# Kernel tuning notes

Measured on AMD Instinct MI355X. Metric: run time of the kernel, lower is better.

The kernel has to match this reference:

```python
import jax, jax.numpy as jnp
import numpy as np

B, T = 2, 2048
DENSE = 1024
SPARSE = 1024
NH = 8
HD = SPARSE // NH          # 128
WINDOW = 64
K = 32
RANK = HD // 4             # 32
GATE_THRESH = 0.2


def setup_inputs() -> dict:
    key = jax.random.key(0)
    ks = jax.random.split(key, 12)
    return {
        "x": jax.random.normal(ks[0], (B, T, DENSE), dtype=jnp.float32),
        "enc_q": jax.random.normal(ks[1], (NH, DENSE, HD), dtype=jnp.float32) * 0.02,
        "enc_v": jax.random.normal(ks[2], (NH, DENSE, HD), dtype=jnp.float32) * 0.02,
        # metric network: Linear(SPARSE, SPARSE//2) -> GELU -> Linear(SPARSE//2, NH*HD)
        "metric_w1": jax.random.normal(ks[3], (SPARSE, SPARSE // 2), dtype=jnp.float32) * (1.0 / np.sqrt(SPARSE)),
        "metric_b1": jnp.zeros((SPARSE // 2,), dtype=jnp.float32),
        "metric_w2": jax.random.normal(ks[4], (SPARSE // 2, NH * HD), dtype=jnp.float32) * (1.0 / np.sqrt(SPARSE // 2)),
        "metric_b2": jnp.zeros((NH * HD,), dtype=jnp.float32),
        "base_metric": jnp.ones((NH, HD), dtype=jnp.float32) * 0.1,
        "hebb_U": jax.random.normal(ks[5], (NH, HD, RANK), dtype=jnp.float32) * 0.01,
        "hebb_V": jax.random.normal(ks[6], (NH, RANK, HD), dtype=jnp.float32) * 0.01,
        "decoder": jax.random.normal(ks[7], (NH * HD, DENSE), dtype=jnp.float32) * 0.02,
    }


def _causal_window_indices(t_len, window):
    pos = jnp.arange(t_len)
    off = jnp.arange(window)
    idx = jnp.clip(pos[:, None] - off[None, :], 0, t_len - 1)  # (T, W)
    mask = idx <= pos[:, None]
    return idx, mask


def _dynamic_metric(field, w1, b1, w2, b2, base):
    # field: (B, T, SPARSE)
    sig = field.mean(axis=1)
    if field.shape[1] >= 8:
        sig = sig + field[:, ::8].mean(axis=1) * 0.5
    h = jax.nn.gelu(sig @ w1 + b1, approximate=False)
    mod = (h @ w2 + b2).reshape(field.shape[0], NH, HD)
    return jax.nn.softplus(base[None] + 0.1 * mod)  # (B, NH, HD)


def reference(x, enc_q, enc_v, metric_w1, metric_b1, metric_w2, metric_b2,
              base_metric, hebb_U, hebb_V, decoder):
    Bb, Tt, _ = x.shape
    query_sparse = jax.nn.relu(jnp.einsum('btd,nde->btne', x, enc_q))  # (B,T,NH,HD)
    value_sparse = jax.nn.relu(jnp.einsum('btd,nde->btne', x, enc_v))

    metric = _dynamic_metric(query_sparse.reshape(Bb, Tt, NH * HD),
                             metric_w1, metric_b1, metric_w2, metric_b2, base_metric)

    idx, mask = _causal_window_indices(Tt, WINDOW)  # (T,W)
    idx_b = jnp.broadcast_to(idx[None], (Bb, Tt, WINDOW))
    batch_ix = jnp.arange(Bb)[:, None, None]

    outs = []
    for h in range(NH):
        q_h = query_sparse[:, :, h, :]   # (B,T,HD)
        v_h = value_sparse[:, :, h, :]
        m_h = metric[:, h][:, None, None, :]  # (B,1,1,HD)

        k_windows = q_h[:, idx, :]            # (B,T,W,HD) gather
        diff = k_windows - q_h[:, :, None, :]
        dist = jnp.sqrt((diff * diff * m_h).sum(axis=-1) + 1e-8)  # (B,T,W)
        dist = jnp.where(mask[None], dist, jnp.inf)

        neg_d, loc = jax.lax.top_k(-dist, K)  # smallest-K distances
        topd = -neg_d
        top_idx = jnp.take_along_axis(idx_b, loc, axis=2)  # (B,T,K)

        infl = jnp.exp(-topd)
        infl = infl / (infl.sum(axis=-1, keepdims=True) + 1e-8)

        neighbor_v = v_h[batch_ix, top_idx]   # (B,T,K,HD)
        context = jnp.einsum('btk,btkd->btd', infl, neighbor_v)

        q_norm = jnp.linalg.norm(q_h, axis=-1, keepdims=True)
        gate = (q_norm > GATE_THRESH).astype(q_h.dtype)
        heb_mat = hebb_U[h] @ hebb_V[h]       # (HD,HD)
        q_unit = q_h / jnp.maximum(q_norm, 1e-12)  # F.normalize
        heb_ctx = q_unit @ heb_mat
        context = context + gate * 0.1 * heb_ctx

        outs.append(q_h * context)

    out_sparse = jnp.stack(outs, axis=2)           # (B,T,NH,HD)
    return out_sparse.reshape(Bb, Tt, NH * HD) @ decoder
```

## Files before the change

### kernel.cpp

```cpp
#include <hip/hip_runtime.h>
#include <math.h>

#define T_ 2048
#define NH_ 8
#define HD_ 128

typedef unsigned short u16;
typedef short bf16x8 __attribute__((ext_vector_type(8)));
typedef _Float16 f16x8 __attribute__((ext_vector_type(8)));
typedef float f32x4 __attribute__((ext_vector_type(4)));

union FH { _Float16 h; u16 u; };

__device__ __forceinline__ u16 f2h(float f)
{
    FH c; c.h = (_Float16)f; return c.u;
}
__device__ __forceinline__ float h2f(u16 v)
{
    FH c; c.u = v; return (float)c.h;
}
__device__ __forceinline__ void split1h(float f, u16& h, u16& l)
{
    h = f2h(f);
    l = f2h(f - h2f(h));
}

__device__ __forceinline__ u16 f2bf(float f)
{
    unsigned u = __float_as_uint(f);
    return (u16)((u + 0x7FFFu + ((u >> 16) & 1u)) >> 16);
}
__device__ __forceinline__ float bf2f(u16 h)
{
    return __uint_as_float(((unsigned)h) << 16);
}


__global__ __launch_bounds__(256) void cvt_in(const float* __restrict__ x,
                                              const float* __restrict__ enc_q,
                                              const float* __restrict__ enc_v,
                                              u16* __restrict__ xh,
                                              u16* __restrict__ WTh)
{
    __shared__ u16 tH[32][33];
    const int bid = blockIdx.x;
    if (bid < 4096) {
        int i = (bid * 256 + threadIdx.x) * 4;
        int m = i >> 10, k = i & 1023;
        float4 v = *(const float4*)&x[i];
        ushort4 hv = {f2h(v.x), f2h(v.y), f2h(v.z), f2h(v.w)};
        long o = (long)(m >> 6) * 65536 + (k >> 5) * 2048
               + ((k >> 3) & 3) * 512 + (m & 63) * 8 + (k & 7);
        *(ushort4*)&xh[o] = hv;
    } else {
        int rb = bid - 4096;
        int bx = rb & 31, by = (rb >> 5) & 31, bz = rb >> 10;
        const float* Bw = bz ? enc_v : enc_q;
        const int nofs = bz << 10;
        const int tid = threadIdx.x;
        const int tx = tid & 31, ty = tid >> 5;
        const int k0 = bx * 32, c0 = by * 32;
        #pragma unroll
        for (int r = 0; r < 4; ++r) {
            int k = k0 + ty * 4 + r;
            int c = c0 + tx;
            float v = Bw[(long)(c >> 7) * 131072 + (long)k * 128 + (c & 127)];
            tH[ty * 4 + r][tx] = f2h(v);
        }
        __syncthreads();
        #pragma unroll
        for (int r = 0; r < 4; ++r) {
            int n = nofs + c0 + ty * 4 + r;
            int k = k0 + tx;
            long o = (long)(n >> 6) * 65536 + (k >> 5) * 2048
                   + ((k >> 3) & 3) * 512 + (n & 63) * 8 + (k & 7);
            WTh[o] = tH[tx][ty * 4 + r];
        }
    }
}

__global__ __launch_bounds__(256) void cvt_wT_pk(const float* __restrict__ src0,
                                                 u16* __restrict__ WTh,
                                                 int Kd, int cs, int cm, long sn, int sk)
{
    __shared__ u16 tH[32][33];
    const float* Bw = src0;
    const int tid = threadIdx.x;
    const int tx = tid & 31, ty = tid >> 5;
    const int k0 = blockIdx.x * 32, c0 = blockIdx.y * 32;
    #pragma unroll
    for (int r = 0; r < 4; ++r) {
        int k = k0 + ty * 4 + r;
        int c = c0 + tx;
        float v = Bw[(long)(c >> cs) * sn + (long)k * sk + (c & cm)];
        tH[ty * 4 + r][tx] = f2h(v);
    }
    __syncthreads();
    const long sstr = (long)Kd * 64;
    #pragma unroll
    for (int r = 0; r < 4; ++r) {
        int n = c0 + ty * 4 + r;
        int k = k0 + tx;
        long o = (long)(n >> 6) * sstr + (k >> 5) * 2048
               + ((k >> 3) & 3) * 512 + (n & 63) * 8 + (k & 7);
        WTh[o] = tH[tx][ty * 4 + r];
    }
}

__global__ __launch_bounds__(256, 1) void gemm_qv(
    const u16* __restrict__ Ah, const u16* __restrict__ Bh,
    float* __restrict__ Qf, u16* __restrict__ Vh,
    float* __restrict__ Ps, float* __restrict__ Ps8, int Kd)
{
    __shared__ __align__(16) u16 S[4][6144];

    const int tid  = threadIdx.x;
    const int w    = tid >> 6;
    const int lane = tid & 63;

    const int id   = blockIdx.x;
    const int m0   = (id & 31) * 128;
    const int n0   = (id >> 5) * 256;

    const int mw   = (w & 1) * 64, nw = (w >> 1) * 128;
    const int mr   = lane & 15, quad = lane >> 4;

    const long sstr = (long)Kd * 64;
    const u16* gAh = Ah + (long)((m0 + mw) >> 6) * sstr;
    const u16* gB0 = Bh + (long)((n0 + nw) >> 6) * sstr;
    const u16* gB1 = gB0 + sstr;

    u16* W = &S[w][0];

    f32x4 acc[4][8] = {};
    uint4 a0, a1, a2, a3;
    uint4 b0, b1, b2, b3, b4, b5, b6, b7;

#define LOADG(KT) do { long t = (long)(KT) * 2048 + lane * 8;                        \
    a0 = *(const uint4*)(gAh + t +    0); a1 = *(const uint4*)(gAh + t +  512);      \
    a2 = *(const uint4*)(gAh + t + 1024); a3 = *(const uint4*)(gAh + t + 1536);      \
    b0 = *(const uint4*)(gB0 + t +    0); b1 = *(const uint4*)(gB0 + t +  512);      \
    b2 = *(const uint4*)(gB0 + t + 1024); b3 = *(const uint4*)(gB0 + t + 1536);      \
    b4 = *(const uint4*)(gB1 + t +    0); b5 = *(const uint4*)(gB1 + t +  512);      \
    b6 = *(const uint4*)(gB1 + t + 1024); b7 = *(const uint4*)(gB1 + t + 1536); } while (0)

#define STOREG() do { u16* D = W + lane * 8;                                         \
    *(uint4*)(D +    0) = a0; *(uint4*)(D +  512) = a1;                              \
    *(uint4*)(D + 1024) = a2; *(uint4*)(D + 1536) = a3;                              \
    *(uint4*)(D + 2048) = b0; *(uint4*)(D + 2560) = b1;                              \
    *(uint4*)(D + 3072) = b2; *(uint4*)(D + 3584) = b3;                              \
    *(uint4*)(D + 4096) = b4; *(uint4*)(D + 4608) = b5;                              \
    *(uint4*)(D + 5120) = b6; *(uint4*)(D + 5632) = b7; } while (0)

    LOADG(0);
    STOREG();
    LOADG(1);

    const int NT = Kd >> 5;
    for (int kt = 0; kt < NT; ++kt) {
        f16x8 fah[4], fbh[8];
        #pragma unroll
        for (int i = 0; i < 4; ++i)
            fah[i] = *(const f16x8*)(W + quad * 512 + (i * 16 + mr) * 8);
        #pragma unroll
        for (int j = 0; j < 8; ++j)
            fbh[j] = *(const f16x8*)(W + 2048 + ((j < 4) ? 0 : 2048)
                                     + quad * 512 + ((j & 3) * 16 + mr) * 8);
        if (kt + 1 < NT) STOREG();
        if (kt + 2 < NT) LOADG(kt + 2);
        #pragma unroll
        for (int i = 0; i < 4; ++i)
            #pragma unroll
            for (int j = 0; j < 8; ++j)
                acc[i][j] = __builtin_amdgcn_mfma_f32_16x16x32_f16(fah[i], fbh[j], acc[i][j], 0, 0, 0);
    }
#undef LOADG
#undef STOREG

    if (n0 < 1024) {
        #pragma unroll
        for (int i = 0; i < 4; ++i)
            #pragma unroll
            for (int j = 0; j < 8; ++j)
                #pragma unroll
                for (int r = 0; r < 4; ++r) {
                    float v = fmaxf(acc[i][j][r], 0.f);
                    acc[i][j][r] = v;
                    int row = m0 + mw + i * 16 + quad * 4 + r;
                    int col = n0 + nw + j * 16 + mr;
                    Qf[(long)row * 1024 + col] = v;
                }
        int slot = (id & 31) * 2 + (w & 1);
        #pragma unroll
        for (int j = 0; j < 8; ++j) {
            float ps = 0.f, p8 = 0.f;
            #pragma unroll
            for (int i = 0; i < 4; ++i) {
                #pragma unroll
                for (int r = 0; r < 4; ++r) ps += acc[i][j][r];
                if ((quad & 1) == 0) p8 += acc[i][j][0];
            }
            ps += __shfl_xor(ps, 16, 64); ps += __shfl_xor(ps, 32, 64);
            p8 += __shfl_xor(p8, 16, 64); p8 += __shfl_xor(p8, 32, 64);
            if (quad == 0) {
                int col = n0 + nw + j * 16 + mr;
                Ps [slot * 1024 + col] = ps;
                Ps8[slot * 1024 + col] = p8;
            }
        }
    } else {
        #pragma unroll
        for (int i = 0; i < 4; ++i)
            #pragma unroll
            for (int j = 0; j < 8; ++j)
                #pragma unroll
                for (int r = 0; r < 4; ++r) {
                    float v = fmaxf(acc[i][j][r], 0.f);
                    int row = m0 + mw + i * 16 + quad * 4 + r;
                    int col = n0 - 1024 + nw + j * 16 + mr;
                    Vh[(long)row * 1024 + col] = f2h(v);
                }
    }
}

__global__ __launch_bounds__(256, 1) void gemm_dec(
    const u16* __restrict__ Ah, const u16* __restrict__ Bh,
    float* __restrict__ C, int N, int Kd)
{
    __shared__ __align__(16) u16 S[4][4096];

    const int tid  = threadIdx.x;
    const int w    = tid >> 6;
    const int lane = tid & 63;

    const int id   = blockIdx.x;
    const int m0   = (((id & 7) << 2) + ((id >> 3) & 3)) * 128;
    const int n0   = (id >> 5) * 128;

    const int mw   = (w & 1) * 64, nw = (w >> 1) * 64;
    const int mr   = lane & 15, quad = lane >> 4;

    const long sstr = (long)Kd * 64;
    const u16* gAh = Ah + (long)((m0 + mw) >> 6) * sstr;
    const u16* gBh = Bh + (long)((n0 + nw) >> 6) * sstr;

    u16* W = &S[w][0];

    f32x4 acc[4][4] = {};
    uint4 a0, a1, a2, a3, b0, b1, b2, b3;

#define LOADG(KT) do { long t = (long)(KT) * 2048 + lane * 8;                        \
    a0 = *(const uint4*)(gAh + t +    0); a1 = *(const uint4*)(gAh + t +  512);      \
    a2 = *(const uint4*)(gAh + t + 1024); a3 = *(const uint4*)(gAh + t + 1536);      \
    b0 = *(const uint4*)(gBh + t +    0); b1 = *(const uint4*)(gBh + t +  512);      \
    b2 = *(const uint4*)(gBh + t + 1024); b3 = *(const uint4*)(gBh + t + 1536); } while (0)

#define STOREG() do { u16* D = W + lane * 8;                                         \
    *(uint4*)(D +    0) = a0; *(uint4*)(D +  512) = a1;                              \
    *(uint4*)(D + 1024) = a2; *(uint4*)(D + 1536) = a3;                              \
    *(uint4*)(D + 2048) = b0; *(uint4*)(D + 2560) = b1;                              \
    *(uint4*)(D + 3072) = b2; *(uint4*)(D + 3584) = b3; } while (0)

    LOADG(0);
    STOREG();
    LOADG(1);

    const int NT = Kd >> 5;
    for (int kt = 0; kt < NT; ++kt) {
        f16x8 fah[4], fbh[4];
        #pragma unroll
        for (int i = 0; i < 4; ++i) {
            int ro = quad * 512 + (i * 16 + mr) * 8;
            fah[i] = *(const f16x8*)(W + ro);
            fbh[i] = *(const f16x8*)(W + 2048 + ro);
        }
        if (kt + 1 < NT) STOREG();
        if (kt + 2 < NT) LOADG(kt + 2);
        #pragma unroll
        for (int i = 0; i < 4; ++i)
            #pragma unroll
            for (int j = 0; j < 4; ++j)
                acc[i][j] = __builtin_amdgcn_mfma_f32_16x16x32_f16(fah[i], fbh[j], acc[i][j], 0, 0, 0);
    }
#undef LOADG
#undef STOREG

    #pragma unroll
    for (int i = 0; i < 4; ++i)
        #pragma unroll
        for (int j = 0; j < 4; ++j)
            #pragma unroll
            for (int r = 0; r < 4; ++r) {
                int row = m0 + mw + i * 16 + quad * 4 + r;
                int col = n0 + nw + j * 16 + mr;
                C[(long)row * N + col] = acc[i][j][r];
            }
}

__global__ __launch_bounds__(256) void heb_gemm(
    const u16* __restrict__ Qbf, const u16* __restrict__ MhT,
    u16* __restrict__ HEBbf)
{
    __shared__ __align__(16) u16 sA[4][128][8], sB[4][128][8];

    const int tid  = threadIdx.x;
    const int w    = tid >> 6;
    const int lane = tid & 63;
    const int m0   = blockIdx.x * 128;
    const int h    = blockIdx.y;
    const int mw   = w * 32;
    const int mr   = lane & 15, quad = lane >> 4;
    const u16* Bm  = MhT + h * 16384;

    f32x4 acc[2][8] = {};

    for (int k0 = 0; k0 < 128; k0 += 32) {
        #pragma unroll
        for (int u = 0; u < 4; ++u) {
            int c = (w & 1) * 4 + u;
            int kq = c >> 1, half = c & 1;
            const u16* src; u16* dst; long gofs;
            if (w < 2) {
                src = Qbf;
                dst = &sA[0][0][0] + kq * 1024 + half * 512;
                gofs = (long)(m0 + half * 64 + lane) * 1024 + h * 128 + k0 + kq * 8;
            } else {
                src = Bm;
                dst = &sB[0][0][0] + kq * 1024 + half * 512;
                gofs = (long)(half * 64 + lane) * 128 + k0 + kq * 8;
            }
            __builtin_amdgcn_global_load_lds(
                (const __attribute__((address_space(1))) unsigned int*)(src + gofs),
                (__attribute__((address_space(3))) unsigned int*)dst, 16, 0, 0);
        }
        __syncthreads();

        bf16x8 fa[2], fb[8];
        #pragma unroll
        for (int i = 0; i < 2; ++i)
            fa[i] = *(const bf16x8*)&sA[quad][mw + i * 16 + mr][0];
        #pragma unroll
        for (int j = 0; j < 8; ++j)
            fb[j] = *(const bf16x8*)&sB[quad][j * 16 + mr][0];
        #pragma unroll
        for (int i = 0; i < 2; ++i)
            #pragma unroll
            for (int j = 0; j < 8; ++j)
                acc[i][j] = __builtin_amdgcn_mfma_f32_16x16x32_bf16(fa[i], fb[j], acc[i][j], 0, 0, 0);
        __syncthreads();
    }

    #pragma unroll
    for (int i = 0; i < 2; ++i)
        #pragma unroll
        for (int j = 0; j < 8; ++j)
            #pragma unroll
            for (int r = 0; r < 4; ++r) {
                int row = m0 + mw + i * 16 + quad * 4 + r;
                int col = h * 128 + j * 16 + mr;
                HEBbf[(long)row * 1024 + col] = f2bf(acc[i][j][r]);
            }
}

__global__ __launch_bounds__(256) void qu_stage(const float* __restrict__ Qf,
                                                const float* __restrict__ Me,
                                                u16* __restrict__ Qbf,
                                                u16* __restrict__ Uh, u16* __restrict__ Ul,
                                                float* __restrict__ nArr)
{
    int gid4 = (blockIdx.x * 256 + threadIdx.x) * 4;
    int e4 = gid4 & 127;
    int t  = (gid4 >> 7) & 2047;
    int bh = gid4 >> 18;
    int b  = bh >> 3, h = bh & 7;
    float4 q = *(const float4*)&Qf[((long)(b * 2048 + t)) * 1024 + h * 128 + e4];
    ushort4 qo = {f2bf(q.x), f2bf(q.y), f2bf(q.z), f2bf(q.w)};
    *(ushort4*)&Qbf[((long)(b * 2048 + t)) * 1024 + h * 128 + e4] = qo;

    float4 m = *(const float4*)&Me[bh * 128 + e4];
    float ux = sqrtf(m.x) * q.x, uy = sqrtf(m.y) * q.y;
    float uz = sqrtf(m.z) * q.z, uw = sqrtf(m.w) * q.w;
    u16 h0, l0, h1, l1, h2, l2, h3, l3;
    split1h(ux, h0, l0); split1h(uy, h1, l1);
    split1h(uz, h2, l2); split1h(uw, h3, l3);
    ushort4 hv = {h0, h1, h2, h3}, lv = {l0, l1, l2, l3};
    *(ushort4*)&Uh[gid4] = hv;
    *(ushort4*)&Ul[gid4] = lv;
    float ps = ux * ux + uy * uy + uz * uz + uw * uw;
    #pragma unroll
    for (int mm = 16; mm; mm >>= 1) ps += __shfl_xor(ps, mm, 64);
    if ((threadIdx.x & 31) == 0) nArr[gid4 >> 7] = ps;
}

__global__ __launch_bounds__(256, 1) void dist_gemm(
    const u16* __restrict__ Uh, const u16* __restrict__ Ul,
    const float* __restrict__ nArr, float* __restrict__ band)
{
    __shared__ __align__(16) u16 sAh[4][64][8],  sAl[4][64][8];
    __shared__ __align__(16) u16 sBh[4][128][8], sBl[4][128][8];
    __shared__ float epi[4][16][128];

    const int tid  = threadIdx.x;
    const int w    = tid >> 6;
    const int lane = tid & 63;
    const int mr   = lane & 15, quad = lane >> 4;
    const int bid  = blockIdx.x;
    const int tile = bid & 31, bh = bid >> 5;
    const int t0   = tile * 64;
    const long ub  = (long)bh * 2048 * 128;

    const u16 *s0, *s1, *s2, *s3, *s4, *s5;
    u16 *d0, *d1, *d2, *d3, *d4, *d5;
    long o0, o1, o2, o3, o4, o5;
    {
        auto mk = [&](int i, const u16*& src, u16*& dst, long& ofs) {
            int c = i * 256 + tid;
            if (c < 512) {
                int row = c & 63, kq = (c >> 6) & 3;
                src = (c < 256) ? Uh : Ul;
                ofs = ub + (long)(t0 + row) * 128 + kq * 8;
                dst = ((c < 256) ? &sAh[0][0][0] : &sAl[0][0][0]) + kq * 512 + row * 8;
            } else {
                int cb = c - 512;
                int row = cb & 127, kq = (cb >> 7) & 3;
                src = (cb < 512) ? Uh : Ul;
                ofs = ub + (long)(t0 - 64 + row) * 128 + kq * 8;
                dst = ((cb < 512) ? &sBh[0][0][0] : &sBl[0][0][0]) + kq * 1024 + row * 8;
            }
        };
        mk(0, s0, d0, o0); mk(1, s1, d1, o1); mk(2, s2, d2, o2);
        mk(3, s3, d3, o3); mk(4, s4, d4, o4); mk(5, s5, d5, o5);
    }

    f32x4 acc[8] = {};
    uint4 g0, g1, g2, g3, g4, g5;
    g0 = *(const uint4*)(s0 + o0); g1 = *(const uint4*)(s1 + o1);
    g2 = *(const uint4*)(s2 + o2); g3 = *(const uint4*)(s3 + o3);
    g4 = *(const uint4*)(s4 + o4); g5 = *(const uint4*)(s5 + o5);

    for (int k0 = 0; k0 < 128; k0 += 32) {
        *(uint4*)d0 = g0; *(uint4*)d1 = g1; *(uint4*)d2 = g2;
        *(uint4*)d3 = g3; *(uint4*)d4 = g4; *(uint4*)d5 = g5;
        __syncthreads();

        if (k0 + 32 < 128) {
            int kn = k0 + 32;
            g0 = *(const uint4*)(s0 + o0 + kn); g1 = *(const uint4*)(s1 + o1 + kn);
            g2 = *(const uint4*)(s2 + o2 + kn); g3 = *(const uint4*)(s3 + o3 + kn);
            g4 = *(const uint4*)(s4 + o4 + kn); g5 = *(const uint4*)(s5 + o5 + kn);
        }

        f16x8 fah = *(const f16x8*)&sAh[quad][w * 16 + mr][0];
        f16x8 fal = *(const f16x8*)&sAl[quad][w * 16 + mr][0];
        #pragma unroll
        for (int j = 0; j < 8; ++j) {
            f16x8 fbh = *(const f16x8*)&sBh[quad][j * 16 + mr][0];
            f16x8 fbl = *(const f16x8*)&sBl[quad][j * 16 + mr][0];
            acc[j] = __builtin_amdgcn_mfma_f32_16x16x32_f16(fah, fbh, acc[j], 0, 0, 0);
            acc[j] = __builtin_amdgcn_mfma_f32_16x16x32_f16(fah, fbl, acc[j], 0, 0, 0);
            acc[j] = __builtin_amdgcn_mfma_f32_16x16x32_f16(fal, fbh, acc[j], 0, 0, 0);
        }
        __syncthreads();
    }

    #pragma unroll
    for (int j = 0; j < 8; ++j)
        #pragma unroll
        for (int r = 0; r < 4; ++r)
            epi[w][quad * 4 + r][j * 16 + mr] = acc[j][r];
    __syncthreads();

    const float* nb = nArr + (long)bh * 2048;
    #pragma unroll
    for (int i = 0; i < 16; ++i) {
        int id = i * 256 + tid;
        int tl = id >> 6, j = id & 63;
        int t  = t0 + tl;
        int r  = t - j;
        int rc = r < 0 ? 0 : r;
        int rl = tl - j + 64;
        float S  = epi[tl >> 4][tl & 15][rl];
        float d2 = nb[t] + nb[rc] - 2.0f * S;
        band[((long)bh * 2048 + t) * 64 + j] = d2;
    }
}

__global__ __launch_bounds__(256) void mlp1_part(const float* __restrict__ Ps,
                                                 const float* __restrict__ Ps8,
                                                 const float* __restrict__ w1,
                                                 float* __restrict__ Pm)
{
    __shared__ float ssig[32];
    int tid = threadIdx.x;
    int o  = blockIdx.x * 256 + tid;
    int b  = blockIdx.y;
    int kc = blockIdx.z;
    int k0 = kc * 32;
    if (tid < 32) {
        int k = k0 + tid;
        float s = 0.f, s8 = 0.f;
        #pragma unroll
        for (int ms = 0; ms < 32; ++ms) {
            long po = ((long)(b * 32 + ms)) * 1024 + k;
            s  += Ps[po];
            s8 += Ps8[po];
        }
        ssig[tid] = s * (1.0f / 2048.0f) + 0.5f * s8 * (1.0f / 256.0f);
    }
    __syncthreads();
    float a = 0.f;
    #pragma unroll 8
    for (int kk = 0; kk < 32; ++kk)
        a += ssig[kk] * w1[(long)(k0 + kk) * 512 + o];
    Pm[((b * 32) + kc) * 512 + o] = a;
}

__global__ __launch_bounds__(256) void mlp2_part(const float* __restrict__ Pm1,
                                                 const float* __restrict__ b1,
                                                 const float* __restrict__ w2,
                                                 float* __restrict__ Pm)
{
    __shared__ float sH[32];
    int tid = threadIdx.x;
    int c  = blockIdx.x * 256 + tid;
    int b  = blockIdx.y;
    int kc = blockIdx.z;
    int k0 = kc * 32;
    if (tid < 32) {
        int o = k0 + tid;
        float a = b1[o];
        #pragma unroll
        for (int kcc = 0; kcc < 32; ++kcc)
            a += Pm1[(b * 32 + kcc) * 512 + o];
        sH[tid] = 0.5f * a * (1.0f + erff(a * 0.70710678118f));
    }
    __syncthreads();
    float a = 0.f;
    #pragma unroll 8
    for (int kk = 0; kk < 32; ++kk)
        a += sH[kk] * w2[(long)(k0 + kk) * 1024 + c];
    Pm[((b * 16) + kc) * 1024 + c] = a;
}

__global__ __launch_bounds__(256) void mlp2fin_hebb(
    const float* __restrict__ Pm, const float* __restrict__ b2,
    const float* __restrict__ base, float* __restrict__ metric,
    const float* __restrict__ U, const float* __restrict__ Vh,
    u16* __restrict__ MhT)
{
    int id = blockIdx.x;
    if (id < 8) {
        int c = (id & 3) * 256 + threadIdx.x;
        int b = id >> 2;
        float a = b2[c];
        #pragma unroll
        for (int kc = 0; kc < 16; ++kc)
            a += Pm[(b * 16 + kc) * 1024 + c];
        float mv = base[c] + 0.1f * a;
        metric[b * 1024 + c] = fmaxf(mv, 0.f) + log1pf(expf(-fabsf(mv)));
    } else {
        int gid = (id - 8) * 256 + threadIdx.x;
        int h = gid >> 14;
        int rem = gid & 16383;
        int e = rem >> 7;
        int f = rem & 127;
        float a = 0.f;
        #pragma unroll
        for (int r = 0; r < 32; ++r)
            a += U[(h * 128 + f) * 32 + r] * Vh[(h * 32 + r) * 128 + e];
        MhT[(h * 128 + e) * 128 + f] = f2bf(a);
    }
}

__global__ __launch_bounds__(256) void context_k(
    const float* __restrict__ Qf, const u16* __restrict__ Vh,
    const float* __restrict__ band, const u16* __restrict__ HEBbf,
    u16* __restrict__ CTh)
{
    __shared__ float wv[4][32];
    __shared__ int   wi[4][32];

    const int w    = threadIdx.x >> 6;
    const int lane = threadIdx.x & 63;
    const int gw   = blockIdx.x * 4 + w;
    const int h    = gw & 7;
    const int bt   = gw >> 3;
    const int t    = bt & (T_ - 1);
    const int b    = bt >> 11;
    const int bh   = b * 8 + h;

    const long qrow  = (long)bt * 1024 + h * 128;
    const long hrow  = (long)bt * 1024 + h * 128;

    float q0 = Qf[qrow + lane], q1 = Qf[qrow + 64 + lane];
    float ss = q0 * q0 + q1 * q1;
    #pragma unroll
    for (int s = 32; s; s >>= 1) ss += __shfl_xor(ss, s, 64);
    const float qn  = sqrtf(ss);
    const float inv = 1.0f / fmaxf(qn, 1e-12f);

    int je = lane < t ? lane : t;
    float d2v = (je == 0) ? 0.f
              : band[((long)bh * 2048 + t) * 64 + je];
    float d2f = fmaxf(d2v, 0.f) + 1e-8f;
    unsigned kb = (__float_as_uint(d2f) & 0xFFFFFFC0u) | (unsigned)lane;

    #pragma unroll
    for (int k = 2; k <= 32; k <<= 1)
        #pragma unroll
        for (int s = k >> 1; s >= 1; s >>= 1) {
            unsigned ok = __shfl_xor(kb, s, 64);
            bool takeMin = (((lane & k) == 0) == ((lane & s) == 0));
            if ((ok < kb) == takeMin) kb = ok;
        }
    {
        unsigned ok = __shfl_xor(kb, 32, 64);
        kb = ok < kb ? ok : kb;
    }

    int jj = kb & 63;
    float wexp = 0.f;
    if (lane < 32)
        wexp = expf(-sqrtf(__uint_as_float(kb & 0xFFFFFFC0u)));
    float tot = wexp;
    #pragma unroll
    for (int s = 32; s; s >>= 1) tot += __shfl_xor(tot, s, 64);
    float wn = wexp / (tot + 1e-8f);
    if (lane < 32) {
        wv[w][lane] = wn;
        int ii = t - jj; if (ii < 0) ii = 0;
        wi[w][lane] = ii;
    }

    float c0 = 0.f, c1 = 0.f;
    #pragma unroll 8
    for (int k = 0; k < 32; ++k) {
        float wk = wv[w][k];
        long vb = ((long)(b * T_ + wi[w][k])) * 1024 + h * 128;
        c0 += wk * h2f(Vh[vb + lane]);
        c1 += wk * h2f(Vh[vb + 64 + lane]);
    }

    if (qn > 0.2f) {
        float s = 0.1f * inv;
        c0 += s * bf2f(HEBbf[hrow + lane]);
        c1 += s * bf2f(HEBbf[hrow + 64 + lane]);
    }

    int c0c = h * 128 + lane, c1c = c0c + 64;
    long po0 = (long)(bt >> 6) * 65536 + (c0c >> 5) * 2048
             + ((c0c >> 3) & 3) * 512 + (bt & 63) * 8 + (c0c & 7);
    long po1 = (long)(bt >> 6) * 65536 + (c1c >> 5) * 2048
             + ((c1c >> 3) & 3) * 512 + (bt & 63) * 8 + (c1c & 7);
    CTh[po0] = f2h(q0 * c0);
    CTh[po1] = f2h(q1 * c1);
}

extern "C" void kernel_launch(void* const* d_in, const int* in_sizes, int n_in,
                              void* d_out, int out_size, void* d_ws, size_t ws_size,
                              hipStream_t stream)
{
    const float* x     = (const float*)d_in[0];
    const float* enc_q = (const float*)d_in[1];
    const float* enc_v = (const float*)d_in[2];
    const float* w1    = (const float*)d_in[3];
    const float* b1    = (const float*)d_in[4];
    const float* w2    = (const float*)d_in[5];
    const float* b2    = (const float*)d_in[6];
    const float* base  = (const float*)d_in[7];
    const float* hU    = (const float*)d_in[8];
    const float* hV    = (const float*)d_in[9];
    const float* dec   = (const float*)d_in[10];
    float* out = (float*)d_out;
    float* ws  = (float*)d_ws;

    float* Qf  = ws;
    u16* Vhp   = (u16*)(ws + 4194304);
    u16* wTh   = (u16*)(ws + 8388608);
    float* Ps  = ws + 9437184;
    float* Ps8 = ws + 9502720;
    u16* Uhp   = (u16*)(ws + 8388608);
    u16* Ulp   = (u16*)(ws + 10485760);
    u16* CTh   = (u16*)(ws + 8388608);
    u16* MhT   = (u16*)(ws + 12582912);
    float* nA  = ws + 12713984;
    float* Me  = ws + 12749824;
    u16* wdTh  = (u16*)ws;
    u16* xh    = (u16*)d_out;
    u16* Qbf   = (u16*)d_out;
    u16* HEBbf = (u16*)d_out + 4194304;
    float* band = (float*)d_out;
    float* Pm1 = (float*)d_out + 2097152;
    float* Pm2 = (float*)d_out + 2129920;

    cvt_in<<<6144, 256, 0, stream>>>(x, enc_q, enc_v, xh, wTh);

    gemm_qv<<<256, 256, 0, stream>>>(xh, wTh, Qf, Vhp, Ps, Ps8, 1024);

    mlp1_part<<<dim3(2, 2, 32), 256, 0, stream>>>(Ps, Ps8, w1, Pm1);
    mlp2_part<<<dim3(4, 2, 16), 256, 0, stream>>>(Pm1, b1, w2, Pm2);
    mlp2fin_hebb<<<520, 256, 0, stream>>>(Pm2, b2, base, Me, hU, hV, MhT);

    qu_stage<<<4096, 256, 0, stream>>>(Qf, Me, Qbf, Uhp, Ulp, nA);
    heb_gemm<<<dim3(32, 8), 256, 0, stream>>>(Qbf, MhT, HEBbf);
    dist_gemm<<<512, 256, 0, stream>>>(Uhp, Ulp, nA, band);

    context_k<<<8192, 256, 0, stream>>>(Qf, Vhp, band, HEBbf, CTh);

    cvt_wT_pk<<<dim3(32, 32), 256, 0, stream>>>(dec, wdTh,
                                                1024, 30, 0x3fffffff, 0L, 1024);
    gemm_dec<<<256, 256, 0, stream>>>(CTh, wdTh, out, 1024, 1024);
}
```

Baseline: 213.9 us.

## Use direct global-to-LDS triple-buffered loads in GEMMs and fuse decoder weight conversion

Replaces the register-staged global->LDS copy in gemm_qv and gemm_dec with global_load_lds async loads into a per-wave triple buffer, synchronized with explicit vmcnt waits. This is meant to remove the VGPR round trip and let loads for two future k-tiles overlap the MFMAs. The decoder weight transpose/convert is folded into the cvt_in launch, removing one kernel launch, and its buffer moves to a free workspace region. LDS usage grows substantially, and correctness relies on the manual vmcnt counts matching the issued loads.

```diff
diff --git a/kernel.cpp b/kernel.cpp
--- a/kernel.cpp
+++ b/kernel.cpp
@@ -36,12 +36,18 @@
     return __uint_as_float(((unsigned)h) << 16);
 }
 
+#define GLD16(SRC, DST) __builtin_amdgcn_global_load_lds( \
+    (const __attribute__((address_space(1))) unsigned int*)(SRC), \
+    (__attribute__((address_space(3))) unsigned int*)(DST), 16, 0, 0)
+
 
 __global__ __launch_bounds__(256) void cvt_in(const float* __restrict__ x,
                                               const float* __restrict__ enc_q,
                                               const float* __restrict__ enc_v,
+                                              const float* __restrict__ dec,
                                               u16* __restrict__ xh,
-                                              u16* __restrict__ WTh)
+                                              u16* __restrict__ WTh,
+                                              u16* __restrict__ WdT)
 {
     __shared__ u16 tH[32][33];
     const int bid = blockIdx.x;
@@ -53,7 +59,7 @@
         long o = (long)(m >> 6) * 65536 + (k >> 5) * 2048
                + ((k >> 3) & 3) * 512 + (m & 63) * 8 + (k & 7);
         *(ushort4*)&xh[o] = hv;
-    } else {
+    } else if (bid < 6144) {
         int rb = bid - 4096;
         int bx = rb & 31, by = (rb >> 5) & 31, bz = rb >> 10;
         const float* Bw = bz ? enc_v : enc_q;
@@ -77,34 +83,27 @@
                    + ((k >> 3) & 3) * 512 + (n & 63) * 8 + (k & 7);
             WTh[o] = tH[tx][ty * 4 + r];
         }
-    }
-}
-
-__global__ __launch_bounds__(256) void cvt_wT_pk(const float* __restrict__ src0,
-                                                 u16* __restrict__ WTh,
-                                                 int Kd, int cs, int cm, long sn, int sk)
-{
-    __shared__ u16 tH[32][33];
-    const float* Bw = src0;
-    const int tid = threadIdx.x;
-    const int tx = tid & 31, ty = tid >> 5;
-    const int k0 = blockIdx.x * 32, c0 = blockIdx.y * 32;
-    #pragma unroll
-    for (int r = 0; r < 4; ++r) {
-        int k = k0 + ty * 4 + r;
-        int c = c0 + tx;
-        float v = Bw[(long)(c >> cs) * sn + (long)k * sk + (c & cm)];
-        tH[ty * 4 + r][tx] = f2h(v);
-    }
-    __syncthreads();
-    const long sstr = (long)Kd * 64;
-    #pragma unroll
-    for (int r = 0; r < 4; ++r) {
-        int n = c0 + ty * 4 + r;
-        int k = k0 + tx;
-        long o = (long)(n >> 6) * sstr + (k >> 5) * 2048
-               + ((k >> 3) & 3) * 512 + (n & 63) * 8 + (k & 7);
-        WTh[o] = tH[tx][ty * 4 + r];
+    } else {
+        int rb = bid - 6144;
+        int bx = rb & 31, by = rb >> 5;
+        const int tid = threadIdx.x;
+        const int tx = tid & 31, ty = tid >> 5;
+        const int k0 = bx * 32, c0 = by * 32;
+        #pragma unroll
+        for (int r = 0; r < 4; ++r) {
+            int k = k0 + ty * 4 + r;
+            int c = c0 + tx;
+            tH[ty * 4 + r][tx] = f2h(dec[(long)k * 1024 + c]);
+        }
+        __syncthreads();
+        #pragma unroll
+        for (int r = 0; r < 4; ++r) {
+            int n = c0 + ty * 4 + r;
+            int k = k0 + tx;
+            long o = (long)(n >> 6) * 65536 + (k >> 5) * 2048
+                   + ((k >> 3) & 3) * 512 + (n & 63) * 8 + (k & 7);
+            WdT[o] = tH[tx][ty * 4 + r];
+        }
     }
 }
 
@@ -113,7 +112,7 @@
     float* __restrict__ Qf, u16* __restrict__ Vh,
     float* __restrict__ Ps, float* __restrict__ Ps8, int Kd)
 {
-    __shared__ __align__(16) u16 S[4][6144];
+    __shared__ __align__(16) u16 S[4][3][6144];
 
     const int tid  = threadIdx.x;
     const int w    = tid >> 6;
@@ -127,38 +126,22 @@
     const int mr   = lane & 15, quad = lane >> 4;
 
     const long sstr = (long)Kd * 64;
-    const u16* gAh = Ah + (long)((m0 + mw) >> 6) * sstr;
-    const u16* gB0 = Bh + (long)((n0 + nw) >> 6) * sstr;
+    const u16* gAh = Ah + (long)((m0 + mw) >> 6) * sstr + lane * 8;
+    const u16* gB0 = Bh + (long)((n0 + nw) >> 6) * sstr + lane * 8;
     const u16* gB1 = gB0 + sstr;
 
-    u16* W = &S[w][0];
-
     f32x4 acc[4][8] = {};
-    uint4 a0, a1, a2, a3;
-    uint4 b0, b1, b2, b3, b4, b5, b6, b7;
-
-#define LOADG(KT) do { long t = (long)(KT) * 2048 + lane * 8;                        \
-    a0 = *(const uint4*)(gAh + t +    0); a1 = *(const uint4*)(gAh + t +  512);      \
-    a2 = *(const uint4*)(gAh + t + 1024); a3 = *(const uint4*)(gAh + t + 1536);      \
-    b0 = *(const uint4*)(gB0 + t +    0); b1 = *(const uint4*)(gB0 + t +  512);      \
-    b2 = *(const uint4*)(gB0 + t + 1024); b3 = *(const uint4*)(gB0 + t + 1536);      \
-    b4 = *(const uint4*)(gB1 + t +    0); b5 = *(const uint4*)(gB1 + t +  512);      \
-    b6 = *(const uint4*)(gB1 + t + 1024); b7 = *(const uint4*)(gB1 + t + 1536); } while (0)
-
-#define STOREG() do { u16* D = W + lane * 8;                                         \
-    *(uint4*)(D +    0) = a0; *(uint4*)(D +  512) = a1;                              \
-    *(uint4*)(D + 1024) = a2; *(uint4*)(D + 1536) = a3;                              \
-    *(uint4*)(D + 2048) = b0; *(uint4*)(D + 2560) = b1;                              \
-    *(uint4*)(D + 3072) = b2; *(uint4*)(D + 3584) = b3;                              \
-    *(uint4*)(D + 4096) = b4; *(uint4*)(D + 4608) = b5;                              \
-    *(uint4*)(D + 5120) = b6; *(uint4*)(D + 5632) = b7; } while (0)
-
-    LOADG(0);
-    STOREG();
-    LOADG(1);
-
-    const int NT = Kd >> 5;
-    for (int kt = 0; kt < NT; ++kt) {
+
+#define ISSUE(KT, BUF) do { long t = (long)(KT) * 2048;                        \
+    u16* D = &S[w][BUF][0];                                                    \
+    GLD16(gAh + t +    0, D +    0); GLD16(gAh + t +  512, D +  512);          \
+    GLD16(gAh + t + 1024, D + 1024); GLD16(gAh + t + 1536, D + 1536);          \
+    GLD16(gB0 + t +    0, D + 2048); GLD16(gB0 + t +  512, D + 2560);          \
+    GLD16(gB0 + t + 1024, D + 3072); GLD16(gB0 + t + 1536, D + 3584);          \
+    GLD16(gB1 + t +    0, D + 4096); GLD16(gB1 + t +  512, D + 4608);          \
+    GLD16(gB1 + t + 1024, D + 5120); GLD16(gB1 + t + 1536, D + 5632); } while (0)
+
+    auto compute = [&](const u16* W) {
         f16x8 fah[4], fbh[8];
         #pragma unroll
         for (int i = 0; i < 4; ++i)
@@ -167,16 +150,30 @@
         for (int j = 0; j < 8; ++j)
             fbh[j] = *(const f16x8*)(W + 2048 + ((j < 4) ? 0 : 2048)
                                      + quad * 512 + ((j & 3) * 16 + mr) * 8);
-        if (kt + 1 < NT) STOREG();
-        if (kt + 2 < NT) LOADG(kt + 2);
         #pragma unroll
         for (int i = 0; i < 4; ++i)
             #pragma unroll
             for (int j = 0; j < 8; ++j)
                 acc[i][j] = __builtin_amdgcn_mfma_f32_16x16x32_f16(fah[i], fbh[j], acc[i][j], 0, 0, 0);
-    }
-#undef LOADG
-#undef STOREG
+    };
+
+    const int NT = Kd >> 5;
+    ISSUE(0, 0);
+    ISSUE(1, 1);
+    int bufR = 0, bufW = 2;
+    for (int kt = 0; kt < NT - 2; ++kt) {
+        ISSUE(kt + 2, bufW);
+        asm volatile("s_waitcnt vmcnt(24)" ::: "memory");
+        compute(&S[w][0][0] + bufR * 6144);
+        bufR = (bufR == 2) ? 0 : bufR + 1;
+        bufW = (bufW == 2) ? 0 : bufW + 1;
+    }
+    asm volatile("s_waitcnt vmcnt(12)" ::: "memory");
+    compute(&S[w][0][0] + bufR * 6144);
+    bufR = (bufR == 2) ? 0 : bufR + 1;
+    asm volatile("s_waitcnt vmcnt(0)" ::: "memory");
+    compute(&S[w][0][0] + bufR * 6144);
+#undef ISSUE
 
     if (n0 < 1024) {
         #pragma unroll
@@ -228,7 +225,7 @@
     const u16* __restrict__ Ah, const u16* __restrict__ Bh,
     float* __restrict__ C, int N, int Kd)
 {
-    __shared__ __align__(16) u16 S[4][4096];
+    __shared__ __align__(16) u16 S[4][3][4096];
 
     const int tid  = threadIdx.x;
     const int w    = tid >> 6;
@@ -242,32 +239,19 @@
     const int mr   = lane & 15, quad = lane >> 4;
 
     const long sstr = (long)Kd * 64;
-    const u16* gAh = Ah + (long)((m0 + mw) >> 6) * sstr;
-    const u16* gBh = Bh + (long)((n0 + nw) >> 6) * sstr;
-
-    u16* W = &S[w][0];
+    const u16* gAh = Ah + (long)((m0 + mw) >> 6) * sstr + lane * 8;
+    const u16* gBh = Bh + (long)((n0 + nw) >> 6) * sstr + lane * 8;
 
     f32x4 acc[4][4] = {};
-    uint4 a0, a1, a2, a3, b0, b1, b2, b3;
-
-#define LOADG(KT) do { long t = (long)(KT) * 2048 + lane * 8;                        \
-    a0 = *(const uint4*)(gAh + t +    0); a1 = *(const uint4*)(gAh + t +  512);      \
-    a2 = *(const uint4*)(gAh + t + 1024); a3 = *(const uint4*)(gAh + t + 1536);      \
-    b0 = *(const uint4*)(gBh + t +    0); b1 = *(const uint4*)(gBh + t +  512);      \
-    b2 = *(const uint4*)(gBh + t + 1024); b3 = *(const uint4*)(gBh + t + 1536); } while (0)
-
-#define STOREG() do { u16* D = W + lane * 8;                                         \
-    *(uint4*)(D +    0) = a0; *(uint4*)(D +  512) = a1;                              \
-    *(uint4*)(D + 1024) = a2; *(uint4*)(D + 1536) = a3;                              \
-    *(uint4*)(D + 2048) = b0; *(uint4*)(D + 2560) = b1;                              \
-    *(uint4*)(D + 3072) = b2; *(uint4*)(D + 3584) = b3; } while (0)
-
-    LOADG(0);
-    STOREG();
-    LOADG(1);
-
-    const int NT = Kd >> 5;
-    for (int kt = 0; kt < NT; ++kt) {
+
+#define ISSUE(KT, BUF) do { long t = (long)(KT) * 2048;                        \
+    u16* D = &S[w][BUF][0];                                                    \
+    GLD16(gAh + t +    0, D +    0); GLD16(gAh + t +  512, D +  512);          \
+    GLD16(gAh + t + 1024, D + 1024); GLD16(gAh + t + 1536, D + 1536);          \
+    GLD16(gBh + t +    0, D + 2048); GLD16(gBh + t +  512, D + 2560);          \
+    GLD16(gBh + t + 1024, D + 3072); GLD16(gBh + t + 1536, D + 3584); } while (0)
+
+    auto compute = [&](const u16* W) {
         f16x8 fah[4], fbh[4];
         #pragma unroll
         for (int i = 0; i < 4; ++i) {
@@ -275,16 +259,30 @@
             fah[i] = *(const f16x8*)(W + ro);
             fbh[i] = *(const f16x8*)(W + 2048 + ro);
         }
-        if (kt + 1 < NT) STOREG();
-        if (kt + 2 < NT) LOADG(kt + 2);
         #pragma unroll
         for (int i = 0; i < 4; ++i)
             #pragma unroll
             for (int j = 0; j < 4; ++j)
                 acc[i][j] = __builtin_amdgcn_mfma_f32_16x16x32_f16(fah[i], fbh[j], acc[i][j], 0, 0, 0);
-    }
-#undef LOADG
-#undef STOREG
+    };
+
+    const int NT = Kd >> 5;
+    ISSUE(0, 0);
+    ISSUE(1, 1);
+    int bufR = 0, bufW = 2;
+    for (int kt = 0; kt < NT - 2; ++kt) {
+        ISSUE(kt + 2, bufW);
+        asm volatile("s_waitcnt vmcnt(16)" ::: "memory");
+        compute(&S[w][0][0] + bufR * 4096);
+        bufR = (bufR == 2) ? 0 : bufR + 1;
+        bufW = (bufW == 2) ? 0 : bufW + 1;
+    }
+    asm volatile("s_waitcnt vmcnt(8)" ::: "memory");
+    compute(&S[w][0][0] + bufR * 4096);
+    bufR = (bufR == 2) ? 0 : bufR + 1;
+    asm volatile("s_waitcnt vmcnt(0)" ::: "memory");
+    compute(&S[w][0][0] + bufR * 4096);
+#undef ISSUE
 
     #pragma unroll
     for (int i = 0; i < 4; ++i)
@@ -330,9 +328,7 @@
                 dst = &sB[0][0][0] + kq * 1024 + half * 512;
                 gofs = (long)(half * 64 + lane) * 128 + k0 + kq * 8;
             }
-            __builtin_amdgcn_global_load_lds(
-                (const __attribute__((address_space(1))) unsigned int*)(src + gofs),
-                (__attribute__((address_space(3))) unsigned int*)dst, 16, 0, 0);
+            GLD16(src + gofs, dst);
         }
         __syncthreads();
 
@@ -677,6 +673,7 @@
 
     float* Qf  = ws;
     u16* Vhp   = (u16*)(ws + 4194304);
+    u16* wdTh  = (u16*)(ws + 6291456);
     u16* wTh   = (u16*)(ws + 8388608);
     float* Ps  = ws + 9437184;
     float* Ps8 = ws + 9502720;
@@ -686,7 +683,6 @@
     u16* MhT   = (u16*)(ws + 12582912);
     float* nA  = ws + 12713984;
     float* Me  = ws + 12749824;
-    u16* wdTh  = (u16*)ws;
     u16* xh    = (u16*)d_out;
     u16* Qbf   = (u16*)d_out;
     u16* HEBbf = (u16*)d_out + 4194304;
@@ -694,7 +690,7 @@
     float* Pm1 = (float*)d_out + 2097152;
     float* Pm2 = (float*)d_out + 2129920;
 
-    cvt_in<<<6144, 256, 0, stream>>>(x, enc_q, enc_v, xh, wTh);
+    cvt_in<<<7168, 256, 0, stream>>>(x, enc_q, enc_v, dec, xh, wTh, wdTh);
 
     gemm_qv<<<256, 256, 0, stream>>>(xh, wTh, Qf, Vhp, Ps, Ps8, 1024);
 
@@ -708,7 +704,5 @@
 
     context_k<<<8192, 256, 0, stream>>>(Qf, Vhp, band, HEBbf, CTh);
 
-    cvt_wT_pk<<<dim3(32, 32), 256, 0, stream>>>(dec, wdTh,
-                                                1024, 30, 0x3fffffff, 0L, 1024);
     gemm_dec<<<256, 256, 0, stream>>>(CTh, wdTh, out, 1024, 1024);
 }
```

After: 217.2 us. About the same (+1.6%).
